# Kernel tuning notes

Measured on AMD Instinct MI355X. Metric: run time of the kernel, lower is better.

The kernel has to match this reference:

```python
import jax, jax.numpy as jnp
import numpy as np

B, S, D, H = 2, 2048, 768, 12
N = D // H  # head dim = 64
NEG = -1e12


def setup_inputs() -> dict:
    key = jax.random.key(0)
    ks = jax.random.split(key, 6)
    scale = 1.0 / np.sqrt(D)
    return {
        "inputs": jax.random.normal(ks[0], (B, S, D), dtype=jnp.float32),
        "masks": jnp.ones((B, S), dtype=jnp.int32),
        "Wq": jax.random.normal(ks[1], (D, D), dtype=jnp.float32) * scale,
        "bq": jnp.zeros((D,), dtype=jnp.float32),
        "Wk": jax.random.normal(ks[2], (D, D), dtype=jnp.float32) * scale,
        "bk": jnp.zeros((D,), dtype=jnp.float32),
        "Wv": jax.random.normal(ks[3], (D, D), dtype=jnp.float32) * scale,
        "bv": jnp.zeros((D,), dtype=jnp.float32),
        "Wo": jax.random.normal(ks[4], (D, D), dtype=jnp.float32) * scale,
        "bo": jnp.zeros((D,), dtype=jnp.float32),
    }


def reference(inputs, masks, Wq, bq, Wk, bk, Wv, bv, Wo, bo):
    # projections: [B,S,D] -> [B,H,S,N]
    def proj(x, W, b):
        y = jnp.einsum('bsd,df->bsf', x, W) + b
        return y.reshape(B, -1, H, N).transpose(0, 2, 1, 3)

    q = proj(inputs, Wq, bq)
    k = proj(inputs, Wk, bk)
    v = proj(inputs, Wv, bv)

    # scores [B,H,S,S]
    a = jnp.einsum('bhqn,bhkn->bhqk', q, k) / jnp.float32(np.sqrt(N))
    m = masks[:, None, None, :]  # [B,1,1,S]
    a = jnp.where(m == 0, jnp.float32(NEG), a)
    a = jax.nn.softmax(a, axis=-1)

    o = jnp.einsum('bhqk,bhkn->bhqn', a, v)  # [B,H,S,N]
    o = o.transpose(0, 2, 1, 3).reshape(B, -1, H * N)
    return jnp.einsum('bsd,df->bsf', o, Wo) + bo
```

## Files before the change

kernel.cpp:

```cpp
#include <hip/hip_runtime.h>
#include <hip/hip_bf16.h>

#define B_ 2
#define S_ 2048
#define D_ 768
#define H_ 12
#define BS_ (B_*S_)
#define NEGL2 -1.44e12f
#define SCALE2 0.18033688f

typedef __bf16 bf16;
typedef __attribute__((ext_vector_type(8))) __bf16 bf16x8;
typedef __attribute__((ext_vector_type(4))) float f32x4;
typedef __attribute__((ext_vector_type(16))) float f32x16;

__device__ inline unsigned pk2(float a, float b) {
    union { unsigned u; __bf16 h[2]; } x;
    x.h[0] = (__bf16)a; x.h[1] = (__bf16)b;
    return x.u;
}

__device__ __forceinline__ void gload16(const void* g, void* l) {
    __builtin_amdgcn_global_load_lds(
        (const __attribute__((address_space(1))) unsigned int*)g,
        (__attribute__((address_space(3))) unsigned int*)l, 16, 0, 0);
}

__global__ __launch_bounds__(256) void prep(const float* __restrict__ x,
                                            const float* __restrict__ Wq,
                                            const float* __restrict__ Wk,
                                            const float* __restrict__ Wv,
                                            const float* __restrict__ Wo,
                                            bf16* __restrict__ Xb,
                                            bf16* __restrict__ Wt0) {
    int id = blockIdx.x;
    if (id < 1536) {
        int i = (id * 256 + threadIdx.x) * 8;
        float4 a = *(const float4*)(x + i);
        float4 b = *(const float4*)(x + i + 4);
        bf16x8 v;
        v[0] = (bf16)a.x; v[1] = (bf16)a.y; v[2] = (bf16)a.z; v[3] = (bf16)a.w;
        v[4] = (bf16)b.x; v[5] = (bf16)b.y; v[6] = (bf16)b.z; v[7] = (bf16)b.w;
        *(bf16x8*)(Xb + i) = v;
        return;
    }
    id -= 1536;
    const int z = id / 144;
    const int rem = id % 144;
    const int by = rem / 12;
    const int bx = rem % 12;
    const float* W = (z == 0) ? Wq : (z == 1) ? Wk : (z == 2) ? Wv : Wo;
    bf16* Wt = Wt0 + (size_t)z * D_ * D_;

    __shared__ float tile[64][68];
    const int r = threadIdx.x >> 2;
    const int c = (threadIdx.x & 3) * 16;

    const float* src = W + (size_t)(by * 64 + r) * D_ + bx * 64 + c;
    *(float4*)&tile[r][c + 0]  = *(const float4*)(src + 0);
    *(float4*)&tile[r][c + 4]  = *(const float4*)(src + 4);
    *(float4*)&tile[r][c + 8]  = *(const float4*)(src + 8);
    *(float4*)&tile[r][c + 12] = *(const float4*)(src + 12);
    __syncthreads();

    bf16 ov[16];
#pragma unroll
    for (int j = 0; j < 16; ++j) ov[j] = (bf16)tile[c + j][r];
    bf16* dst = Wt + (size_t)(bx * 64 + r) * D_ + by * 64 + c;
    *(bf16x8*)dst = *(bf16x8*)&ov[0];
    *(bf16x8*)(dst + 8) = *(bf16x8*)&ov[8];
}

__global__ __launch_bounds__(256) void gemm_qkv(const bf16* __restrict__ A,
                                                const bf16* __restrict__ Bt,
                                                const float* __restrict__ bq,
                                                const float* __restrict__ bk,
                                                const float* __restrict__ bv,
                                                bf16* __restrict__ Qo,
                                                bf16* __restrict__ Ko,
                                                bf16* __restrict__ Vo) {
    constexpr int K = 768;
    __shared__ __align__(16) bf16 As[64 * 64];
    __shared__ __align__(16) bf16 Bs[128 * 64];
    const int bm = blockIdx.x, bn = blockIdx.y;
    const int t = threadIdx.x;
    const int lane = t & 63, wid = t >> 6;
    const int wm = wid >> 1, wn = wid & 1;
    f32x4 acc[2][4] = {};

    const char* gA = (const char*)(A + (size_t)(bm * 64) * K);
    const char* gB = (const char*)(Bt + (size_t)(bn * 128) * K);
    const int srow = wid * 8 + (lane >> 3);
    const int chg = ((lane & 7) ^ (lane >> 3)) * 16;

    for (int kt = 0; kt < 12; ++kt) {
        __syncthreads();
#pragma unroll
        for (int c = 0; c < 2; ++c)
            gload16(gA + (size_t)(c * 32 + srow) * (K * 2) + kt * 128 + chg,
                    (char*)As + c * 4096 + wid * 1024);
#pragma unroll
        for (int c = 0; c < 4; ++c)
            gload16(gB + (size_t)(c * 32 + srow) * (K * 2) + kt * 128 + chg,
                    (char*)Bs + c * 4096 + wid * 1024);
        asm volatile("s_waitcnt vmcnt(0)");
        __syncthreads();

#pragma unroll
        for (int kb = 0; kb < 2; ++kb) {
            const int chunk = ((kb * 4 + (lane >> 4)) ^ (lane & 7)) * 16;
            bf16x8 aF[2], bF[4];
#pragma unroll
            for (int mf = 0; mf < 2; ++mf)
                aF[mf] = *(const bf16x8*)((const char*)As + (wm * 32 + mf * 16 + (lane & 15)) * 128 + chunk);
#pragma unroll
            for (int nf = 0; nf < 4; ++nf)
                bF[nf] = *(const bf16x8*)((const char*)Bs + (wn * 64 + nf * 16 + (lane & 15)) * 128 + chunk);
#pragma unroll
            for (int mf = 0; mf < 2; ++mf)
#pragma unroll
                for (int nf = 0; nf < 4; ++nf)
                    acc[mf][nf] = __builtin_amdgcn_mfma_f32_16x16x32_bf16(aF[mf], bF[nf], acc[mf][nf], 0, 0, 0);
        }
    }

    const int mid = bn / 6;
    const float* bias = (mid == 0) ? bq : (mid == 1) ? bk : bv;
#pragma unroll
    for (int mf = 0; mf < 2; ++mf) {
#pragma unroll
        for (int nf = 0; nf < 4; ++nf) {
#pragma unroll
            for (int r = 0; r < 4; ++r) {
                int row = bm * 64 + wm * 32 + mf * 16 + (lane >> 4) * 4 + r;
                int lc = (bn - mid * 6) * 128 + wn * 64 + nf * 16 + (lane & 15);
                float v = acc[mf][nf][r] + bias[lc];
                if (mid == 0) {
                    Qo[(size_t)row * D_ + lc] = (bf16)(v * SCALE2);
                } else if (mid == 1) {
                    Ko[(size_t)row * D_ + lc] = (bf16)v;
                } else {
                    int bb = row >> 11, s = row & 2047, hh = lc >> 6, nn = lc & 63;
                    Vo[(size_t)(((bb * H_ + hh) << 6) + nn) * S_ + s] = (bf16)v;
                }
            }
        }
    }
}

__global__ __launch_bounds__(256) void gemm_out(const bf16* __restrict__ A,
                                                const bf16* __restrict__ Bt,
                                                const float* __restrict__ bias,
                                                float* __restrict__ Cout) {
    constexpr int K = 768;
    __shared__ __align__(16) bf16 As[32 * 64];
    __shared__ __align__(16) bf16 Bs[128 * 64];
    const int bm = blockIdx.x, bn = blockIdx.y;
    const int t = threadIdx.x;
    const int lane = t & 63, wid = t >> 6;
    const int wm = wid >> 1, wn = wid & 1;
    f32x4 acc[4] = {};

    const char* gA = (const char*)(A + (size_t)(bm * 32) * K);
    const char* gB = (const char*)(Bt + (size_t)(bn * 128) * K);
    const int srow = wid * 8 + (lane >> 3);
    const int chg = ((lane & 7) ^ (lane >> 3)) * 16;

    for (int kt = 0; kt < 12; ++kt) {
        __syncthreads();
        gload16(gA + (size_t)srow * (K * 2) + kt * 128 + chg,
                (char*)As + wid * 1024);
#pragma unroll
        for (int c = 0; c < 4; ++c)
            gload16(gB + (size_t)(c * 32 + srow) * (K * 2) + kt * 128 + chg,
                    (char*)Bs + c * 4096 + wid * 1024);
        asm volatile("s_waitcnt vmcnt(0)");
        __syncthreads();

#pragma unroll
        for (int kb = 0; kb < 2; ++kb) {
            const int chunk = ((kb * 4 + (lane >> 4)) ^ (lane & 7)) * 16;
            bf16x8 aF = *(const bf16x8*)((const char*)As + (wm * 16 + (lane & 15)) * 128 + chunk);
            bf16x8 bF[4];
#pragma unroll
            for (int nf = 0; nf < 4; ++nf)
                bF[nf] = *(const bf16x8*)((const char*)Bs + (wn * 64 + nf * 16 + (lane & 15)) * 128 + chunk);
#pragma unroll
            for (int nf = 0; nf < 4; ++nf)
                acc[nf] = __builtin_amdgcn_mfma_f32_16x16x32_bf16(aF, bF[nf], acc[nf], 0, 0, 0);
        }
    }

#pragma unroll
    for (int nf = 0; nf < 4; ++nf)
#pragma unroll
        for (int r = 0; r < 4; ++r) {
            int row = bm * 32 + wm * 16 + (lane >> 4) * 4 + r;
            int col = bn * 128 + wn * 64 + nf * 16 + (lane & 15);
            Cout[(size_t)row * D_ + col] = acc[nf][r] + bias[col];
        }
}

__global__ __launch_bounds__(256, 3) void attn_fwd10(const bf16* __restrict__ Qs,
                                                     const bf16* __restrict__ Kg,
                                                     const bf16* __restrict__ Vt,
                                                     const int* __restrict__ masks,
                                                     bf16* __restrict__ Oa) {
    __shared__ __align__(16) char Sbuf[2][16384];
    __shared__ float Lr[2][64];

    const int qt = blockIdx.x, bh = blockIdx.y;
    const int b = bh / H_, h = bh % H_;
    const int t = threadIdx.x;
    const int lane = t & 63, w = t >> 6;
    const int lo = lane & 31, hi = lane >> 5;
    const int half = w >> 1;
    const int qs = w & 1;
    const int role = w & 1;

    unsigned long long mflags;
    {
        const int* mb = masks + b * S_ + half * 1024 + lane * 16;
        int anyz = 0;
#pragma unroll
        for (int u = 0; u < 4; ++u) {
            int4 mv = *(const int4*)(mb + u * 4);
            anyz |= (!mv.x) | (!mv.y) | (!mv.z) | (!mv.w);
        }
        mflags = __ballot(anyz != 0);
    }

    bf16x8 bQ[4];
    {
        const bf16* qp = Qs + (size_t)(b * S_ + qt * 64 + qs * 32 + lo) * D_ + h * 64 + 8 * hi;
#pragma unroll
        for (int kb = 0; kb < 4; ++kb) bQ[kb] = *(const bf16x8*)(qp + 16 * kb);
    }

    const int srow = lane >> 3;
    const int scolS = ((lane & 7) * 16) ^ ((srow & 7) << 4);
    const char* gsrc;
    size_t cstride, tstep;
    if (role == 0) {
        gsrc = (const char*)Kg + ((size_t)(b * S_ + half * 1024 + srow) * D_ + h * 64) * 2 + scolS;
        cstride = (size_t)8 * D_ * 2;
        tstep = (size_t)64 * D_ * 2;
    } else {
        gsrc = (const char*)Vt + ((size_t)(bh * 64 + srow) * S_ + half * 1024) * 2 + scolS;
        cstride = (size_t)8 * S_ * 2;
        tstep = 128;
    }
    char* dst = &Sbuf[half][0] + role * 8192 + lane * 16;
    const char* Kh = &Sbuf[half][0];
    const char* Vh = Kh + 8192;

    bf16x8 sreg[8];
#pragma unroll
    for (int j = 0; j < 8; ++j) sreg[j] = *(const bf16x8*)(gsrc + j * cstride);

    f32x16 oo[2] = {};
    float lrun = 0.f;

#pragma unroll 1
    for (int kt = 0; kt < 16; ++kt) {
        __syncthreads();
#pragma unroll
        for (int j = 0; j < 8; ++j) *(bf16x8*)(dst + j * 1024) = sreg[j];
        __syncthreads();
        if (kt < 15) {
            const char* p = gsrc + (size_t)(kt + 1) * tstep;
#pragma unroll
            for (int j = 0; j < 8; ++j) sreg[j] = *(const bf16x8*)(p + j * cstride);
        }

        const bool mk = (mflags >> (4 * kt)) & 0xFULL;
        float lsum = 0.f;
#pragma unroll
        for (int kb2 = 0; kb2 < 2; ++kb2) {
            const int row = kb2 * 32 + lo;
            const int rsw = (row & 7) << 4;
            f32x16 sa = {};
            __builtin_amdgcn_s_setprio(1);
#pragma unroll
            for (int kb = 0; kb < 4; ++kb) {
                bf16x8 aK = *(const bf16x8*)(Kh + row * 128 + ((kb * 32 + hi * 16) ^ rsw));
                sa = __builtin_amdgcn_mfma_f32_32x32x16_bf16(aK, bQ[kb], sa, 0, 0, 0);
            }
            __builtin_amdgcn_s_setprio(0);
            float pp[16];
            if (!mk) {
#pragma unroll
                for (int r = 0; r < 16; ++r) pp[r] = __builtin_amdgcn_exp2f(sa[r]);
            } else {
#pragma unroll
                for (int r = 0; r < 16; ++r) {
                    int kv = half * 1024 + kt * 64 + kb2 * 32 + (r & 3) + 8 * (r >> 2) + 4 * hi;
                    float madd = masks[b * S_ + kv] ? 0.f : NEGL2;
                    pp[r] = __builtin_amdgcn_exp2f(sa[r] + madd);
                }
            }
            float s8[8];
#pragma unroll
            for (int i = 0; i < 8; ++i) s8[i] = pp[i] + pp[i + 8];
            lsum += ((s8[0] + s8[1]) + (s8[2] + s8[3])) + ((s8[4] + s8[5]) + (s8[6] + s8[7]));

#pragma unroll
            for (int ks2 = 0; ks2 < 2; ++ks2) {
                const float* q8 = pp + ks2 * 8;
                unsigned u0 = pk2(q8[0], q8[1]);
                unsigned u1 = pk2(q8[2], q8[3]);
                unsigned u2 = pk2(q8[4], q8[5]);
                unsigned u3 = pk2(q8[6], q8[7]);
                asm("v_permlane32_swap_b32 %0, %1" : "+v"(u0), "+v"(u2));
                asm("v_permlane32_swap_b32 %0, %1" : "+v"(u1), "+v"(u3));
                union { unsigned u[4]; bf16x8 v; } pa;
                pa.u[0] = u0; pa.u[1] = u1; pa.u[2] = u2; pa.u[3] = u3;
                const int ks = kb2 * 2 + ks2;
                __builtin_amdgcn_s_setprio(1);
#pragma unroll
                for (int nb = 0; nb < 2; ++nb) {
                    const int vr = nb * 32 + lo;
                    bf16x8 aV = *(const bf16x8*)(Vh + vr * 128 +
                                                 ((ks * 32 + hi * 16) ^ ((vr & 7) << 4)));
                    oo[nb] = __builtin_amdgcn_mfma_f32_32x32x16_bf16(aV, pa.v, oo[nb], 0, 0, 0);
                }
                __builtin_amdgcn_s_setprio(0);
            }
        }
        lrun += lsum + __shfl_xor(lsum, 32, 64);
    }

    __syncthreads();
    float* mbuf = (float*)&Sbuf[0][0];
    if (w >= 2) {
        float* d = mbuf + qs * 2048;
#pragma unroll
        for (int nb = 0; nb < 2; ++nb)
#pragma unroll
            for (int r = 0; r < 16; ++r)
                d[(nb * 16 + r) * 64 + lane] = oo[nb][r];
        Lr[qs][lane] = lrun;
    }
    __syncthreads();
    if (w < 2) {
        const float* s = mbuf + qs * 2048;
#pragma unroll
        for (int nb = 0; nb < 2; ++nb)
#pragma unroll
            for (int r = 0; r < 16; ++r)
                oo[nb][r] += s[(nb * 16 + r) * 64 + lane];
        float inv = 1.f / (lrun + Lr[qs][lane]);

        char* ot = (char*)&Sbuf[1][0] + qs * 8192;
#pragma unroll
        for (int nb = 0; nb < 2; ++nb)
#pragma unroll
            for (int tq = 0; tq < 4; ++tq) {
                int n0 = tq * 8 + hi * 4 + nb * 32;
                *(unsigned*)(ot + lo * 144 + n0 * 2) =
                    pk2(oo[nb][tq * 4 + 0] * inv, oo[nb][tq * 4 + 1] * inv);
                *(unsigned*)(ot + lo * 144 + n0 * 2 + 4) =
                    pk2(oo[nb][tq * 4 + 2] * inv, oo[nb][tq * 4 + 3] * inv);
            }
#pragma unroll
        for (int pass = 0; pass < 4; ++pass) {
            int chunk = hi + pass * 2;
            bf16x8 vv = *(const bf16x8*)(ot + lo * 144 + chunk * 16);
            *(bf16x8*)(Oa + (size_t)(b * S_ + qt * 64 + qs * 32 + lo) * D_ + h * 64 + chunk * 8) = vv;
        }
    }
}

extern "C" void kernel_launch(void* const* d_in, const int* in_sizes, int n_in,
                              void* d_out, int out_size, void* d_ws, size_t ws_size,
                              hipStream_t stream) {
    (void)in_sizes; (void)n_in; (void)out_size; (void)ws_size;
    const float* x  = (const float*)d_in[0];
    const int* masks = (const int*)d_in[1];
    const float* Wq = (const float*)d_in[2];
    const float* bq = (const float*)d_in[3];
    const float* Wk = (const float*)d_in[4];
    const float* bk = (const float*)d_in[5];
    const float* Wv = (const float*)d_in[6];
    const float* bv = (const float*)d_in[7];
    const float* Wo = (const float*)d_in[8];
    const float* bo = (const float*)d_in[9];
    float* out = (float*)d_out;

    char* ws = (char*)d_ws;
    size_t off = 0;
    auto alloc = [&](size_t bytes) {
        void* p = ws + off;
        off += (bytes + 255) & ~(size_t)255;
        return p;
    };
    bf16* Xb  = (bf16*)alloc((size_t)BS_ * D_ * 2);
    bf16* Wqt = (bf16*)alloc((size_t)D_ * D_ * 2);
    bf16* Wkt = (bf16*)alloc((size_t)D_ * D_ * 2);
    bf16* Wvt = (bf16*)alloc((size_t)D_ * D_ * 2);
    bf16* Wot = (bf16*)alloc((size_t)D_ * D_ * 2);
    bf16* Qb  = (bf16*)alloc((size_t)BS_ * D_ * 2);
    bf16* Kb2 = (bf16*)alloc((size_t)BS_ * D_ * 2);
    bf16* Vtb = (bf16*)alloc((size_t)BS_ * D_ * 2);
    bf16* Ab  = (bf16*)alloc((size_t)BS_ * D_ * 2);
    (void)Wkt; (void)Wvt;

    prep<<<dim3(1536 + 576), 256, 0, stream>>>(x, Wq, Wk, Wv, Wo, Xb, Wqt);

    gemm_qkv<<<dim3(64, 18), 256, 0, stream>>>(Xb, Wqt, bq, bk, bv, Qb, Kb2, Vtb);

    attn_fwd10<<<dim3(32, 24), 256, 0, stream>>>(Qb, Kb2, Vtb, masks, Ab);

    gemm_out<<<dim3(128, 6), 256, 0, stream>>>(Ab, Wot, bo, out);
}
```

Measured before the change: 95.56 us.

## Split attention KV range across four warps with per-warp async LDS loads

```diff
diff --git a/kernel.cpp b/kernel.cpp
--- a/kernel.cpp
+++ b/kernel.cpp
@@ -201,172 +201,225 @@
         }
 }
 
-__global__ __launch_bounds__(256, 3) void attn_fwd10(const bf16* __restrict__ Qs,
+__global__ __launch_bounds__(256, 3) void attn_fwd11(const bf16* __restrict__ Qs,
                                                      const bf16* __restrict__ Kg,
                                                      const bf16* __restrict__ Vt,
                                                      const int* __restrict__ masks,
                                                      bf16* __restrict__ Oa) {
-    __shared__ __align__(16) char Sbuf[2][16384];
-    __shared__ float Lr[2][64];
+    __shared__ __align__(16) char Sbuf[4][8192];
+    __shared__ float Lr[4][2][32];
 
     const int qt = blockIdx.x, bh = blockIdx.y;
     const int b = bh / H_, h = bh % H_;
     const int t = threadIdx.x;
     const int lane = t & 63, w = t >> 6;
     const int lo = lane & 31, hi = lane >> 5;
-    const int half = w >> 1;
-    const int qs = w & 1;
-    const int role = w & 1;
 
     unsigned long long mflags;
     {
-        const int* mb = masks + b * S_ + half * 1024 + lane * 16;
-        int anyz = 0;
-#pragma unroll
-        for (int u = 0; u < 4; ++u) {
-            int4 mv = *(const int4*)(mb + u * 4);
-            anyz |= (!mv.x) | (!mv.y) | (!mv.z) | (!mv.w);
-        }
-        mflags = __ballot(anyz != 0);
-    }
-
-    bf16x8 bQ[4];
+        const int* mb = masks + b * S_ + w * 512 + lane * 8;
+        int4 m0 = *(const int4*)mb, m1 = *(const int4*)(mb + 4);
+        int anyz = (!m0.x) | (!m0.y) | (!m0.z) | (!m0.w) |
+                   (!m1.x) | (!m1.y) | (!m1.z) | (!m1.w);
+        mflags = __ballot(anyz);
+    }
+
+    bf16x8 bQ0[4], bQ1[4];
     {
-        const bf16* qp = Qs + (size_t)(b * S_ + qt * 64 + qs * 32 + lo) * D_ + h * 64 + 8 * hi;
-#pragma unroll
-        for (int kb = 0; kb < 4; ++kb) bQ[kb] = *(const bf16x8*)(qp + 16 * kb);
-    }
-
-    const int srow = lane >> 3;
-    const int scolS = ((lane & 7) * 16) ^ ((srow & 7) << 4);
-    const char* gsrc;
-    size_t cstride, tstep;
-    if (role == 0) {
-        gsrc = (const char*)Kg + ((size_t)(b * S_ + half * 1024 + srow) * D_ + h * 64) * 2 + scolS;
-        cstride = (size_t)8 * D_ * 2;
-        tstep = (size_t)64 * D_ * 2;
-    } else {
-        gsrc = (const char*)Vt + ((size_t)(bh * 64 + srow) * S_ + half * 1024) * 2 + scolS;
-        cstride = (size_t)8 * S_ * 2;
-        tstep = 128;
-    }
-    char* dst = &Sbuf[half][0] + role * 8192 + lane * 16;
-    const char* Kh = &Sbuf[half][0];
-    const char* Vh = Kh + 8192;
-
-    bf16x8 sreg[8];
-#pragma unroll
-    for (int j = 0; j < 8; ++j) sreg[j] = *(const bf16x8*)(gsrc + j * cstride);
-
-    f32x16 oo[2] = {};
-    float lrun = 0.f;
+        const bf16* qp0 = Qs + (size_t)(b * S_ + qt * 64 + lo) * D_ + h * 64 + 8 * hi;
+        const bf16* qp1 = qp0 + (size_t)32 * D_;
+#pragma unroll
+        for (int kb = 0; kb < 4; ++kb) {
+            bQ0[kb] = *(const bf16x8*)(qp0 + 16 * kb);
+            bQ1[kb] = *(const bf16x8*)(qp1 + 16 * kb);
+        }
+    }
+
+    const char* baseK = (const char*)Kg +
+        ((size_t)(b * S_ + w * 512 + (lane >> 3)) * D_ + h * 64) * 2 +
+        (((lane & 7) * 16) ^ ((lane >> 3) << 4));
+    const char* baseV = (const char*)Vt +
+        ((size_t)(bh * 64 + (lane >> 2)) * S_ + w * 512) * 2 +
+        (((lane & 3) * 16) ^ (((lane >> 2) & 3) << 4));
+    char* Kq = &Sbuf[w][0];
+    char* Vq = Kq + 4096;
+
+    f32x16 oo0[2] = {};
+    f32x16 oo1[2] = {};
+    float lrun0 = 0.f, lrun1 = 0.f;
 
 #pragma unroll 1
     for (int kt = 0; kt < 16; ++kt) {
-        __syncthreads();
-#pragma unroll
-        for (int j = 0; j < 8; ++j) *(bf16x8*)(dst + j * 1024) = sreg[j];
-        __syncthreads();
-        if (kt < 15) {
-            const char* p = gsrc + (size_t)(kt + 1) * tstep;
-#pragma unroll
-            for (int j = 0; j < 8; ++j) sreg[j] = *(const bf16x8*)(p + j * cstride);
-        }
+        asm volatile("s_waitcnt lgkmcnt(0)" ::: "memory");
+        __builtin_amdgcn_sched_barrier(0);
+        const char* pK = baseK + (size_t)kt * (32 * D_ * 2);
+#pragma unroll
+        for (int j = 0; j < 4; ++j)
+            gload16(pK + (size_t)j * (8 * D_ * 2), Kq + j * 1024);
+        const char* pV = baseV + (size_t)kt * 64;
+#pragma unroll
+        for (int j = 0; j < 4; ++j)
+            gload16(pV + (size_t)j * (16 * S_ * 2), Vq + j * 1024);
+        asm volatile("s_waitcnt vmcnt(0)" ::: "memory");
+        __builtin_amdgcn_sched_barrier(0);
 
         const bool mk = (mflags >> (4 * kt)) & 0xFULL;
-        float lsum = 0.f;
-#pragma unroll
-        for (int kb2 = 0; kb2 < 2; ++kb2) {
-            const int row = kb2 * 32 + lo;
-            const int rsw = (row & 7) << 4;
-            f32x16 sa = {};
+        f32x16 sa0 = {}, sa1 = {};
+        __builtin_amdgcn_s_setprio(1);
+#pragma unroll
+        for (int kb = 0; kb < 4; ++kb) {
+            bf16x8 aK = *(const bf16x8*)(Kq + lo * 128 + ((kb * 32 + hi * 16) ^ ((lo & 7) << 4)));
+            sa0 = __builtin_amdgcn_mfma_f32_32x32x16_bf16(aK, bQ0[kb], sa0, 0, 0, 0);
+            sa1 = __builtin_amdgcn_mfma_f32_32x32x16_bf16(aK, bQ1[kb], sa1, 0, 0, 0);
+        }
+        __builtin_amdgcn_s_setprio(0);
+
+        float pp0[16], pp1[16];
+        if (!mk) {
+#pragma unroll
+            for (int r = 0; r < 16; ++r) {
+                pp0[r] = __builtin_amdgcn_exp2f(sa0[r]);
+                pp1[r] = __builtin_amdgcn_exp2f(sa1[r]);
+            }
+        } else {
+#pragma unroll
+            for (int r = 0; r < 16; ++r) {
+                int kv = w * 512 + kt * 32 + (r & 3) + 8 * (r >> 2) + 4 * hi;
+                float madd = masks[b * S_ + kv] ? 0.f : NEGL2;
+                pp0[r] = __builtin_amdgcn_exp2f(sa0[r] + madd);
+                pp1[r] = __builtin_amdgcn_exp2f(sa1[r] + madd);
+            }
+        }
+        {
+            float s8[8];
+#pragma unroll
+            for (int i = 0; i < 8; ++i) s8[i] = pp0[i] + pp0[i + 8];
+            float ls = ((s8[0] + s8[1]) + (s8[2] + s8[3])) + ((s8[4] + s8[5]) + (s8[6] + s8[7]));
+            lrun0 += ls + __shfl_xor(ls, 32, 64);
+#pragma unroll
+            for (int i = 0; i < 8; ++i) s8[i] = pp1[i] + pp1[i + 8];
+            ls = ((s8[0] + s8[1]) + (s8[2] + s8[3])) + ((s8[4] + s8[5]) + (s8[6] + s8[7]));
+            lrun1 += ls + __shfl_xor(ls, 32, 64);
+        }
+
+#pragma unroll
+        for (int ks2 = 0; ks2 < 2; ++ks2) {
+            const float* q80 = pp0 + ks2 * 8;
+            unsigned a0 = pk2(q80[0], q80[1]), a1 = pk2(q80[2], q80[3]);
+            unsigned a2 = pk2(q80[4], q80[5]), a3 = pk2(q80[6], q80[7]);
+            asm("v_permlane32_swap_b32 %0, %1" : "+v"(a0), "+v"(a2));
+            asm("v_permlane32_swap_b32 %0, %1" : "+v"(a1), "+v"(a3));
+            union { unsigned u[4]; bf16x8 v; } pa0;
+            pa0.u[0] = a0; pa0.u[1] = a1; pa0.u[2] = a2; pa0.u[3] = a3;
+            const float* q81 = pp1 + ks2 * 8;
+            unsigned c0 = pk2(q81[0], q81[1]), c1 = pk2(q81[2], q81[3]);
+            unsigned c2 = pk2(q81[4], q81[5]), c3 = pk2(q81[6], q81[7]);
+            asm("v_permlane32_swap_b32 %0, %1" : "+v"(c0), "+v"(c2));
+            asm("v_permlane32_swap_b32 %0, %1" : "+v"(c1), "+v"(c3));
+            union { unsigned u[4]; bf16x8 v; } pa1;
+            pa1.u[0] = c0; pa1.u[1] = c1; pa1.u[2] = c2; pa1.u[3] = c3;
             __builtin_amdgcn_s_setprio(1);
 #pragma unroll
-            for (int kb = 0; kb < 4; ++kb) {
-                bf16x8 aK = *(const bf16x8*)(Kh + row * 128 + ((kb * 32 + hi * 16) ^ rsw));
-                sa = __builtin_amdgcn_mfma_f32_32x32x16_bf16(aK, bQ[kb], sa, 0, 0, 0);
+            for (int nb = 0; nb < 2; ++nb) {
+                const int vr = nb * 32 + lo;
+                bf16x8 aV = *(const bf16x8*)(Vq + vr * 64 +
+                                             ((ks2 * 32 + hi * 16) ^ ((vr & 3) << 4)));
+                oo0[nb] = __builtin_amdgcn_mfma_f32_32x32x16_bf16(aV, pa0.v, oo0[nb], 0, 0, 0);
+                oo1[nb] = __builtin_amdgcn_mfma_f32_32x32x16_bf16(aV, pa1.v, oo1[nb], 0, 0, 0);
             }
             __builtin_amdgcn_s_setprio(0);
-            float pp[16];
-            if (!mk) {
-#pragma unroll
-                for (int r = 0; r < 16; ++r) pp[r] = __builtin_amdgcn_exp2f(sa[r]);
-            } else {
-#pragma unroll
-                for (int r = 0; r < 16; ++r) {
-                    int kv = half * 1024 + kt * 64 + kb2 * 32 + (r & 3) + 8 * (r >> 2) + 4 * hi;
-                    float madd = masks[b * S_ + kv] ? 0.f : NEGL2;
-                    pp[r] = __builtin_amdgcn_exp2f(sa[r] + madd);
-                }
-            }
-            float s8[8];
-#pragma unroll
-            for (int i = 0; i < 8; ++i) s8[i] = pp[i] + pp[i + 8];
-            lsum += ((s8[0] + s8[1]) + (s8[2] + s8[3])) + ((s8[4] + s8[5]) + (s8[6] + s8[7]));
-
-#pragma unroll
-            for (int ks2 = 0; ks2 < 2; ++ks2) {
-                const float* q8 = pp + ks2 * 8;
-                unsigned u0 = pk2(q8[0], q8[1]);
-                unsigned u1 = pk2(q8[2], q8[3]);
-                unsigned u2 = pk2(q8[4], q8[5]);
-                unsigned u3 = pk2(q8[6], q8[7]);
-                asm("v_permlane32_swap_b32 %0, %1" : "+v"(u0), "+v"(u2));
-                asm("v_permlane32_swap_b32 %0, %1" : "+v"(u1), "+v"(u3));
-                union { unsigned u[4]; bf16x8 v; } pa;
-                pa.u[0] = u0; pa.u[1] = u1; pa.u[2] = u2; pa.u[3] = u3;
-                const int ks = kb2 * 2 + ks2;
-                __builtin_amdgcn_s_setprio(1);
-#pragma unroll
-                for (int nb = 0; nb < 2; ++nb) {
-                    const int vr = nb * 32 + lo;
-                    bf16x8 aV = *(const bf16x8*)(Vh + vr * 128 +
-                                                 ((ks * 32 + hi * 16) ^ ((vr & 7) << 4)));
-                    oo[nb] = __builtin_amdgcn_mfma_f32_32x32x16_bf16(aV, pa.v, oo[nb], 0, 0, 0);
-                }
-                __builtin_amdgcn_s_setprio(0);
-            }
-        }
-        lrun += lsum + __shfl_xor(lsum, 32, 64);
-    }
-
+        }
+    }
+
+    Lr[w][0][lo] = lrun0;
+    Lr[w][1][lo] = lrun1;
     __syncthreads();
-    float* mbuf = (float*)&Sbuf[0][0];
+    float* Mb = (float*)&Sbuf[0][0];
     if (w >= 2) {
-        float* d = mbuf + qs * 2048;
-#pragma unroll
-        for (int nb = 0; nb < 2; ++nb)
-#pragma unroll
-            for (int r = 0; r < 16; ++r)
-                d[(nb * 16 + r) * 64 + lane] = oo[nb][r];
-        Lr[qs][lane] = lrun;
+        float* d = Mb + (w - 2) * 4096;
+#pragma unroll
+        for (int nb = 0; nb < 2; ++nb)
+#pragma unroll
+            for (int r = 0; r < 16; ++r) {
+                d[((0 * 2 + nb) * 16 + r) * 64 + lane] = oo0[nb][r];
+                d[((1 * 2 + nb) * 16 + r) * 64 + lane] = oo1[nb][r];
+            }
     }
     __syncthreads();
     if (w < 2) {
-        const float* s = mbuf + qs * 2048;
+        const float* s = Mb + w * 4096;
+#pragma unroll
+        for (int nb = 0; nb < 2; ++nb)
+#pragma unroll
+            for (int r = 0; r < 16; ++r) {
+                oo0[nb][r] += s[((0 * 2 + nb) * 16 + r) * 64 + lane];
+                oo1[nb][r] += s[((1 * 2 + nb) * 16 + r) * 64 + lane];
+            }
+    }
+    __syncthreads();
+    if (w == 1) {
 #pragma unroll
         for (int nb = 0; nb < 2; ++nb)
 #pragma unroll
             for (int r = 0; r < 16; ++r)
-                oo[nb][r] += s[(nb * 16 + r) * 64 + lane];
-        float inv = 1.f / (lrun + Lr[qs][lane]);
-
-        char* ot = (char*)&Sbuf[1][0] + qs * 8192;
+                Mb[(nb * 16 + r) * 64 + lane] = oo0[nb][r];
+    }
+    if (w == 0) {
+#pragma unroll
+        for (int nb = 0; nb < 2; ++nb)
+#pragma unroll
+            for (int r = 0; r < 16; ++r)
+                Mb[2048 + (nb * 16 + r) * 64 + lane] = oo1[nb][r];
+    }
+    __syncthreads();
+
+    if (w == 0) {
+#pragma unroll
+        for (int nb = 0; nb < 2; ++nb)
+#pragma unroll
+            for (int r = 0; r < 16; ++r)
+                oo0[nb][r] += Mb[(nb * 16 + r) * 64 + lane];
+        float inv = 1.f / (Lr[0][0][lo] + Lr[1][0][lo] + Lr[2][0][lo] + Lr[3][0][lo]);
+        char* ot = (char*)&Sbuf[2][0];
 #pragma unroll
         for (int nb = 0; nb < 2; ++nb)
 #pragma unroll
             for (int tq = 0; tq < 4; ++tq) {
                 int n0 = tq * 8 + hi * 4 + nb * 32;
                 *(unsigned*)(ot + lo * 144 + n0 * 2) =
-                    pk2(oo[nb][tq * 4 + 0] * inv, oo[nb][tq * 4 + 1] * inv);
+                    pk2(oo0[nb][tq * 4 + 0] * inv, oo0[nb][tq * 4 + 1] * inv);
                 *(unsigned*)(ot + lo * 144 + n0 * 2 + 4) =
-                    pk2(oo[nb][tq * 4 + 2] * inv, oo[nb][tq * 4 + 3] * inv);
+                    pk2(oo0[nb][tq * 4 + 2] * inv, oo0[nb][tq * 4 + 3] * inv);
             }
 #pragma unroll
         for (int pass = 0; pass < 4; ++pass) {
             int chunk = hi + pass * 2;
             bf16x8 vv = *(const bf16x8*)(ot + lo * 144 + chunk * 16);
-            *(bf16x8*)(Oa + (size_t)(b * S_ + qt * 64 + qs * 32 + lo) * D_ + h * 64 + chunk * 8) = vv;
+            *(bf16x8*)(Oa + (size_t)(b * S_ + qt * 64 + lo) * D_ + h * 64 + chunk * 8) = vv;
+        }
+    } else if (w == 1) {
+#pragma unroll
+        for (int nb = 0; nb < 2; ++nb)
+#pragma unroll
+            for (int r = 0; r < 16; ++r)
+                oo1[nb][r] += Mb[2048 + (nb * 16 + r) * 64 + lane];
+        float inv = 1.f / (Lr[0][1][lo] + Lr[1][1][lo] + Lr[2][1][lo] + Lr[3][1][lo]);
+        char* ot = (char*)&Sbuf[3][0];
+#pragma unroll
+        for (int nb = 0; nb < 2; ++nb)
+#pragma unroll
+            for (int tq = 0; tq < 4; ++tq) {
+                int n0 = tq * 8 + hi * 4 + nb * 32;
+                *(unsigned*)(ot + lo * 144 + n0 * 2) =
+                    pk2(oo1[nb][tq * 4 + 0] * inv, oo1[nb][tq * 4 + 1] * inv);
+                *(unsigned*)(ot + lo * 144 + n0 * 2 + 4) =
+                    pk2(oo1[nb][tq * 4 + 2] * inv, oo1[nb][tq * 4 + 3] * inv);
+            }
+#pragma unroll
+        for (int pass = 0; pass < 4; ++pass) {
+            int chunk = hi + pass * 2;
+            bf16x8 vv = *(const bf16x8*)(ot + lo * 144 + chunk * 16);
+            *(bf16x8*)(Oa + (size_t)(b * S_ + qt * 64 + 32 + lo) * D_ + h * 64 + chunk * 8) = vv;
         }
     }
 }
@@ -409,7 +462,7 @@
 
     gemm_qkv<<<dim3(64, 18), 256, 0, stream>>>(Xb, Wqt, bq, bk, bv, Qb, Kb2, Vtb);
 
-    attn_fwd10<<<dim3(32, 24), 256, 0, stream>>>(Qb, Kb2, Vtb, masks, Ab);
+    attn_fwd11<<<dim3(32, 24), 256, 0, stream>>>(Qb, Kb2, Vtb, masks, Ab);
 
     gemm_out<<<dim3(128, 6), 256, 0, stream>>>(Ab, Wot, bo, out);
 }
```

After: 105.7 us. +10.6%, slower.
